# Performance work log

Measured on AMD Instinct MI355X. Metric: run time of the kernel, lower is better.

The kernel has to match this reference:

```python
import jax, jax.numpy as jnp
import numpy as np

ADAPT_RATE = 0.05


def setup_inputs() -> dict:
    key = jax.random.key(0)
    k1, k2, k3 = jax.random.split(key, 3)
    B, T, DIN, DOUT = 64, 256, 1024, 1024
    x = jax.random.normal(k1, (B, T, DIN), dtype=jnp.float32)
    W = jax.random.normal(k2, (DOUT, DIN), dtype=jnp.float32) / np.sqrt(DIN)
    b = jax.random.normal(k3, (DOUT,), dtype=jnp.float32) * 0.01
    threshold = jnp.ones((DOUT,), dtype=jnp.float32)
    return {"x": x, "W": W, "b": b, "threshold": threshold}


def reference(x, W, b, threshold):
    # Precompute the per-timestep linear once as a single big GEMM: [B,T,O]
    pre = jnp.einsum('bti,oi->bto', x, W) + b
    B, T, O = pre.shape

    def step(carry, pre_t):
        mem, thr = carry
        mem = mem + pre_t                       # membrane accumulate [B,O]
        s = (mem >= thr).astype(pre_t.dtype)    # hard threshold spike
        # adaptive threshold: in-place .data update in torch (no grad path)
        thr = thr + ADAPT_RATE * (s.mean(axis=0) - 0.5)
        mem = mem * (1.0 - s)                   # reset where spiked
        return (mem, thr), s

    mem0 = jnp.zeros((B, O), dtype=x.dtype)
    (_, _), spikes = jax.lax.scan(step, (mem0, threshold), jnp.swapaxes(pre, 0, 1))
    return jnp.swapaxes(spikes, 0, 1)  # [B,T,O]
```

## Files before the change

kernel.cpp:

```cpp
#include <hip/hip_runtime.h>

#define B_ 64
#define T_ 256
#define DIN_ 1024
#define DOUT_ 1024

typedef int v4i  __attribute__((ext_vector_type(4)));
typedef int v16i __attribute__((ext_vector_type(16)));

#define PRE_BYTES 134217728ULL
#define XS_BYTES  83886080ULL
#define WSL_BYTES 5242880ULL
#define SPM_BYTES 2097152ULL

__global__ __launch_bounds__(256) void snn_split_x(
    const float* __restrict__ x, char* __restrict__ xs)
{
    const int W    = blockIdx.x * 4 + (threadIdx.x >> 6);
    const int lane = threadIdx.x & 63;
    const int mt = W & 1, kt = (W >> 1) & 31, t0 = W >> 6;
    const int m = lane & 31, kh = lane >> 5;
    const int b = mt * 32 + m;

    const float* src = x + ((size_t)b * T_ + t0) * DIN_ + kt * 32 + kh * 16;
    float f[16];
    *(float4*)(f)      = *(const float4*)(src);
    *(float4*)(f + 4)  = *(const float4*)(src + 4);
    *(float4*)(f + 8)  = *(const float4*)(src + 8);
    *(float4*)(f + 12) = *(const float4*)(src + 12);

    unsigned pk[4][4];
#pragma unroll
    for (int s = 0; s < 4; ++s)
        pk[s][0] = pk[s][1] = pk[s][2] = pk[s][3] = 0u;
#pragma unroll
    for (int j = 0; j < 16; ++j) {
        float v = f[j] * 0.125f;
#pragma unroll
        for (int s = 0; s < 4; ++s) {
            const float ml = (s == 0) ? 64.f : 128.f;
            const float sv = __builtin_rintf(v * ml);
            v = v * ml - sv;
            const int iv = (int)sv;
            pk[s][j >> 2] |= ((unsigned)iv & 0xffu) << ((j & 3) * 8);
        }
    }
#pragma unroll
    for (int s = 0; s < 4; ++s) {
        char* dst = xs + (size_t)(((s * 256 + t0) * 32 + kt) * 2 + mt) * 1024
                       + lane * 16;
        *(uint4*)dst = make_uint4(pk[s][0], pk[s][1], pk[s][2], pk[s][3]);
    }
}

__global__ __launch_bounds__(256) void snn_split_w(
    const float* __restrict__ Wt, char* __restrict__ wsl)
{
    const int W    = blockIdx.x * 4 + (threadIdx.x >> 6);
    const int lane = threadIdx.x & 63;
    const int kt = W & 31, ot = W >> 5;
    const int n = lane & 31, kh = lane >> 5;
    const int o = ot * 32 + n;

    const float* src = Wt + (size_t)o * DIN_ + kt * 32 + kh * 16;
    float f[16];
    *(float4*)(f)      = *(const float4*)(src);
    *(float4*)(f + 4)  = *(const float4*)(src + 4);
    *(float4*)(f + 8)  = *(const float4*)(src + 8);
    *(float4*)(f + 12) = *(const float4*)(src + 12);

    unsigned pk[4][4];
#pragma unroll
    for (int s = 0; s < 4; ++s)
        pk[s][0] = pk[s][1] = pk[s][2] = pk[s][3] = 0u;
#pragma unroll
    for (int j = 0; j < 16; ++j) {
        float v = f[j] * 4.0f;
#pragma unroll
        for (int s = 0; s < 4; ++s) {
            const float ml = (s == 0) ? 64.f : 128.f;
            const float sv = __builtin_rintf(v * ml);
            v = v * ml - sv;
            const int iv = (int)sv;
            pk[s][j >> 2] |= ((unsigned)iv & 0xffu) << ((j & 3) * 8);
        }
    }
#pragma unroll
    for (int s = 0; s < 4; ++s) {
        char* dst = wsl + (size_t)((s * 32 + ot) * 32 + kt) * 1024 + lane * 16;
        *(uint4*)dst = make_uint4(pk[s][0], pk[s][1], pk[s][2], pk[s][3]);
    }
}

__global__ __launch_bounds__(256, 3) void snn_gemm_i8(
    const char* __restrict__ xs, const char* __restrict__ wsl,
    const float* __restrict__ bias, double* __restrict__ pre)
{
    const int t0 = blockIdx.x >> 4;
    const int oc = blockIdx.x & 15;
    const int tid = threadIdx.x;
    const int lane = tid & 63;
    const int ws = __builtin_amdgcn_readfirstlane(tid >> 6);
    const int wm = ws >> 1;
    const int wo = ws & 1;
    const int lo = lane * 16;

    v16i acc[4];
#pragma unroll
    for (int g = 0; g < 4; ++g)
#pragma unroll
        for (int r = 0; r < 16; ++r) acc[g][r] = 0;

    const char* ab = xs  + (size_t)(t0 * 64 + wm) * 1024 + lo;
    const char* bb = wsl + (size_t)((oc * 2 + wo) * 32) * 1024 + lo;

    v4i aP[4], bP[4], aQ[4], bQ[4];

#define LOAD_A(R, KT)                                                          \
    do { _Pragma("unroll")                                                     \
        for (int s = 0; s < 4; ++s)                                            \
            R[s] = *(const v4i*)(ab + (size_t)s * 16777216 +                   \
                                 (size_t)(KT) * 2048);                         \
    } while (0)
#define LOAD_B(R, KT)                                                          \
    do { _Pragma("unroll")                                                     \
        for (int s = 0; s < 4; ++s)                                            \
            R[s] = *(const v4i*)(bb + (size_t)s * 1048576 +                    \
                                 (size_t)(KT) * 1024);                         \
    } while (0)
#define MFMA10(A, B)                                                           \
    do {                                                                       \
        __builtin_amdgcn_s_setprio(1);                                         \
        acc[3] = __builtin_amdgcn_mfma_i32_32x32x32_i8(A[0], B[3], acc[3],0,0,0);\
        acc[2] = __builtin_amdgcn_mfma_i32_32x32x32_i8(A[0], B[2], acc[2],0,0,0);\
        acc[1] = __builtin_amdgcn_mfma_i32_32x32x32_i8(A[0], B[1], acc[1],0,0,0);\
        acc[3] = __builtin_amdgcn_mfma_i32_32x32x32_i8(A[1], B[2], acc[3],0,0,0);\
        acc[2] = __builtin_amdgcn_mfma_i32_32x32x32_i8(A[1], B[1], acc[2],0,0,0);\
        acc[1] = __builtin_amdgcn_mfma_i32_32x32x32_i8(A[1], B[0], acc[1],0,0,0);\
        acc[3] = __builtin_amdgcn_mfma_i32_32x32x32_i8(A[2], B[1], acc[3],0,0,0);\
        acc[2] = __builtin_amdgcn_mfma_i32_32x32x32_i8(A[2], B[0], acc[2],0,0,0);\
        acc[0] = __builtin_amdgcn_mfma_i32_32x32x32_i8(A[0], B[0], acc[0],0,0,0);\
        acc[3] = __builtin_amdgcn_mfma_i32_32x32x32_i8(A[3], B[0], acc[3],0,0,0);\
        __builtin_amdgcn_s_setprio(0);                                         \
    } while (0)

    LOAD_A(aP, 0); LOAD_B(bP, 0);
    for (int ks = 0; ks < 15; ++ks) {
        const int kt = 2 * ks;
        LOAD_A(aQ, kt + 1); LOAD_B(bQ, kt + 1);
        MFMA10(aP, bP);
        LOAD_A(aP, kt + 2); LOAD_B(bP, kt + 2);
        MFMA10(aQ, bQ);
    }
    LOAD_A(aQ, 31); LOAD_B(bQ, 31);
    MFMA10(aP, bP);
    MFMA10(aQ, bQ);

#undef LOAD_A
#undef LOAD_B
#undef MFMA10

    const int n = lane & 31, lh = lane >> 5;
    const int o = oc * 64 + wo * 32 + n;
    const double bv = (double)bias[o];
    double* dst = pre + ((size_t)t0 * DOUT_ + o) * 64 + wm * 32;
#pragma unroll
    for (int r = 0; r < 16; ++r) {
        const int row = (r & 3) + 8 * (r >> 2) + 4 * lh;
        double v = (double)acc[3][r];
        v = v * 0.0078125 + (double)acc[2][r];
        v = v * 0.0078125 + (double)acc[1][r];
        v = v * 0.0078125 + (double)acc[0][r];
        dst[row] = v * 0x1p-11 + bv;
    }
}

__global__ __launch_bounds__(256, 2) void snn_gemm_fb(
    const float* __restrict__ x, const float* __restrict__ W,
    const float* __restrict__ bias, double* __restrict__ pre)
{
    __shared__ float smem[2][8 * 72 + 8 * 256];
    const int t0 = blockIdx.x & 255;
    const int o0 = blockIdx.x >> 8;
    const int tid = threadIdx.x;
    const int to = tid & 31;
    const int tb = tid >> 5;

    double acc[8][8];
#pragma unroll
    for (int i = 0; i < 8; ++i)
#pragma unroll
        for (int j = 0; j < 8; ++j) acc[i][j] = 0.0;

    const int arow = tid >> 2;
    const int ak2  = (tid & 3) * 2;
    const float* xg = x + (size_t)(t0 + 256 * arow) * DIN_ + ak2;
    const float* wg = W + (size_t)(o0 * 256 + tid) * DIN_;

    float2 f2  = *(const float2*)(xg);
    float4 bq0 = *(const float4*)(wg);
    float4 bq1 = *(const float4*)(wg + 4);

    for (int kc = 0; kc < DIN_ / 8; ++kc) {
        float* base = smem[kc & 1];
        float (*AsF)[72]  = (float(*)[72])base;
        float (*BsF)[256] = (float(*)[256])(base + 8 * 72);
        AsF[ak2 + 0][arow] = f2.x;
        AsF[ak2 + 1][arow] = f2.y;
        BsF[0][tid] = bq0.x;  BsF[1][tid] = bq0.y;
        BsF[2][tid] = bq0.z;  BsF[3][tid] = bq0.w;
        BsF[4][tid] = bq1.x;  BsF[5][tid] = bq1.y;
        BsF[6][tid] = bq1.z;  BsF[7][tid] = bq1.w;
        __syncthreads();
        if (kc + 1 < DIN_ / 8) {
            f2  = *(const float2*)(xg + (kc + 1) * 8);
            bq0 = *(const float4*)(wg + (kc + 1) * 8);
            bq1 = *(const float4*)(wg + (kc + 1) * 8 + 4);
        }
#pragma unroll
        for (int k = 0; k < 8; ++k) {
            const float4 af0 = *(const float4*)&AsF[k][tb * 8];
            const float4 af1 = *(const float4*)&AsF[k][tb * 8 + 4];
            const float4 bf0 = *(const float4*)&BsF[k][to * 4];
            const float4 bf1 = *(const float4*)&BsF[k][128 + to * 4];
            double a[8], b[8];
            a[0] = (double)af0.x; a[1] = (double)af0.y;
            a[2] = (double)af0.z; a[3] = (double)af0.w;
            a[4] = (double)af1.x; a[5] = (double)af1.y;
            a[6] = (double)af1.z; a[7] = (double)af1.w;
            b[0] = (double)bf0.x; b[1] = (double)bf0.y;
            b[2] = (double)bf0.z; b[3] = (double)bf0.w;
            b[4] = (double)bf1.x; b[5] = (double)bf1.y;
            b[6] = (double)bf1.z; b[7] = (double)bf1.w;
#pragma unroll
            for (int i = 0; i < 8; ++i)
#pragma unroll
                for (int j = 0; j < 8; ++j)
                    acc[i][j] += a[i] * b[j];
        }
        __syncthreads();
    }

    double biasd[8];
#pragma unroll
    for (int j = 0; j < 8; ++j)
        biasd[j] = (double)bias[o0 * 256 + (j >> 2) * 128 + to * 4 + (j & 3)];
    double (*trans)[67] = (double(*)[67])smem[0];
    for (int c = 0; c < 16; ++c) {
        __syncthreads();
        const int j4  = c >> 3;
        const int tlo = (c & 7) * 4;
        if (to >= tlo && to < tlo + 4) {
#pragma unroll
            for (int p4 = 0; p4 < 4; ++p4) {
                const int r = (to - tlo) * 4 + p4;
                const int j = j4 * 4 + p4;
#pragma unroll
                for (int i = 0; i < 8; ++i)
                    trans[r][tb * 8 + i] = acc[i][j] + biasd[j];
            }
        }
        __syncthreads();
#pragma unroll
        for (int q = 0; q < 4; ++q) {
            const int idx = tid + 256 * q;
            const int b  = idx & 63;
            const int oc = idx >> 6;
            pre[(size_t)(t0 * DOUT_ + o0 * 256 + c * 16 + oc) * 64 + b] = trans[oc][b];
        }
    }
}

#define SCAN_LOAD(PV, TB)                                                      \
    do {                                                                       \
        _Pragma("unroll")                                                      \
        for (int j = 0; j < 16; ++j)                                           \
            PV[j] = p[(size_t)((TB) + j) * (DOUT_ * 64)];                      \
    } while (0)

#define SCAN_STEP(PV, TB)                                                      \
    do {                                                                       \
        _Pragma("unroll")                                                      \
        for (int j = 0; j < 16; ++j) {                                         \
            mem += PV[j];                                                      \
            const bool s = (mem >= thr);                                       \
            const unsigned long long msk = __ballot(s);                        \
            thr += 0.05 * ((double)__popcll(msk) * (1.0 / 64.0) - 0.5);        \
            if (spM) {                                                         \
                if (lane == 0) spM[(size_t)((TB) + j) * DOUT_ + o] = msk;      \
            } else {                                                           \
                outD[(size_t)lane * (T_ * DOUT_) +                             \
                     (size_t)((TB) + j) * DOUT_ + o] = s ? 1.0f : 0.0f;        \
            }                                                                  \
            mem = s ? 0.0 : mem;                                               \
        }                                                                      \
    } while (0)

__global__ __launch_bounds__(256) void snn_scan(
    const double* __restrict__ pre, const float* __restrict__ thr_in,
    unsigned long long* __restrict__ spM, float* __restrict__ outD)
{
    const int wid  = (blockIdx.x * blockDim.x + threadIdx.x) >> 6;
    const int lane = threadIdx.x & 63;
    if (wid >= DOUT_) return;
    const int o = wid;

    double mem = 0.0;
    double thr = (double)thr_in[o];
    const double* p = pre + (size_t)o * 64 + lane;

    double pvA[16], pvB[16];
    SCAN_LOAD(pvA, 0);
    for (int t = 0; t < T_; t += 32) {
        if (t + 16 < T_) SCAN_LOAD(pvB, t + 16);
        SCAN_STEP(pvA, t);
        if (t + 32 < T_) SCAN_LOAD(pvA, t + 32);
        SCAN_STEP(pvB, t + 16);
    }
}

__global__ __launch_bounds__(256) void snn_expand(
    const unsigned long long* __restrict__ spM, float* __restrict__ out)
{
    const int idx = blockIdx.x * 256 + threadIdx.x;
    const int og = idx & 255;
    const int t  = idx >> 8;
    const unsigned long long* mp = spM + (size_t)t * DOUT_ + og * 4;
    const unsigned long long m0 = mp[0], m1 = mp[1], m2 = mp[2], m3 = mp[3];
    float* op = out + (size_t)t * DOUT_ + og * 4;
#pragma unroll
    for (int b = 0; b < 64; ++b) {
        float4 v;
        v.x = (float)((m0 >> b) & 1ULL);
        v.y = (float)((m1 >> b) & 1ULL);
        v.z = (float)((m2 >> b) & 1ULL);
        v.w = (float)((m3 >> b) & 1ULL);
        *(float4*)(op + (size_t)b * (T_ * DOUT_)) = v;
    }
}

extern "C" void kernel_launch(void* const* d_in, const int* in_sizes, int n_in,
                              void* d_out, int out_size, void* d_ws, size_t ws_size,
                              hipStream_t stream) {
    const float* x    = (const float*)d_in[0];
    const float* W    = (const float*)d_in[1];
    const float* bias = (const float*)d_in[2];
    const float* thr  = (const float*)d_in[3];
    float* out = (float*)d_out;

    double* pre = (double*)d_ws;
    const size_t need = PRE_BYTES + XS_BYTES + WSL_BYTES + SPM_BYTES;

    if (ws_size >= need) {
        char* xs  = (char*)d_ws + PRE_BYTES;
        char* wsl = xs + XS_BYTES;
        unsigned long long* spM = (unsigned long long*)(wsl + WSL_BYTES);
        snn_split_x<<<4096, 256, 0, stream>>>(x, xs);
        snn_split_w<<<256, 256, 0, stream>>>(W, wsl);
        snn_gemm_i8<<<4096, 256, 0, stream>>>(xs, wsl, bias, pre);
        snn_scan<<<256, 256, 0, stream>>>(pre, thr, spM, nullptr);
        snn_expand<<<256, 256, 0, stream>>>(spM, out);
    } else {
        const bool two_stage = (ws_size >= PRE_BYTES + SPM_BYTES);
        unsigned long long* spM =
            two_stage ? (unsigned long long*)((char*)d_ws + PRE_BYTES) : nullptr;
        snn_gemm_fb<<<1024, 256, 0, stream>>>(x, W, bias, pre);
        snn_scan<<<256, 256, 0, stream>>>(pre, thr, spM, two_stage ? nullptr : out);
        if (two_stage)
            snn_expand<<<1024, 256, 0, stream>>>(spM, out);
    }
}
```

Measured before the change: 372.7 us.

## Stage W slices through LDS via async global_load_lds with triple buffering

The int8 GEMM now loads B (weight) tiles cooperatively into a three-stage LDS ring buffer using global_load_lds async copies, instead of each wave loading its own B fragments from global memory. Waves that share the same weight columns now read them from LDS, which cuts redundant global and L2 traffic. In exchange it adds a workgroup barrier and manual vmcnt waits every k-step. It also uses 24KB of LDS per block, which may limit occupancy.

```diff
diff --git a/kernel.cpp b/kernel.cpp
--- a/kernel.cpp
+++ b/kernel.cpp
@@ -12,6 +12,12 @@
 #define XS_BYTES  83886080ULL
 #define WSL_BYTES 5242880ULL
 #define SPM_BYTES 2097152ULL
+
+__device__ __forceinline__ void async_copy16(const void* g, void* l) {
+    __builtin_amdgcn_global_load_lds(
+        (const __attribute__((address_space(1))) void*)g,
+        (__attribute__((address_space(3))) void*)l, 16, 0, 0);
+}
 
 __global__ __launch_bounds__(256) void snn_split_x(
     const float* __restrict__ x, char* __restrict__ xs)
@@ -96,6 +102,7 @@
     const char* __restrict__ xs, const char* __restrict__ wsl,
     const float* __restrict__ bias, double* __restrict__ pre)
 {
+    __shared__ __align__(16) char ldsB[3][8 * 1024];
     const int t0 = blockIdx.x >> 4;
     const int oc = blockIdx.x & 15;
     const int tid = threadIdx.x;
@@ -111,10 +118,15 @@
 #pragma unroll
         for (int r = 0; r < 16; ++r) acc[g][r] = 0;
 
-    const char* ab = xs  + (size_t)(t0 * 64 + wm) * 1024 + lo;
-    const char* bb = wsl + (size_t)((oc * 2 + wo) * 32) * 1024 + lo;
-
-    v4i aP[4], bP[4], aQ[4], bQ[4];
+    const char* ab = xs + (size_t)(t0 * 64 + wm) * 1024 + lo;
+
+    const int c0 = ws * 2, c1 = ws * 2 + 1;
+    const char* sgB0 = wsl + (size_t)(c0 & 3) * 1048576
+                           + (size_t)(oc * 2 + (c0 >> 2)) * 32768 + lo;
+    const char* sgB1 = wsl + (size_t)(c1 & 3) * 1048576
+                           + (size_t)(oc * 2 + (c1 >> 2)) * 32768 + lo;
+
+    v4i aP[4], aQ[4];
 
 #define LOAD_A(R, KT)                                                          \
     do { _Pragma("unroll")                                                     \
@@ -122,11 +134,10 @@
             R[s] = *(const v4i*)(ab + (size_t)s * 16777216 +                   \
                                  (size_t)(KT) * 2048);                         \
     } while (0)
-#define LOAD_B(R, KT)                                                          \
-    do { _Pragma("unroll")                                                     \
-        for (int s = 0; s < 4; ++s)                                            \
-            R[s] = *(const v4i*)(bb + (size_t)s * 1048576 +                    \
-                                 (size_t)(KT) * 1024);                         \
+#define STAGE(JB, BUF)                                                         \
+    do {                                                                       \
+        async_copy16(sgB0 + (size_t)(JB) * 1024, &ldsB[BUF][c0 * 1024]);       \
+        async_copy16(sgB1 + (size_t)(JB) * 1024, &ldsB[BUF][c1 * 1024]);       \
     } while (0)
 #define MFMA10(A, B)                                                           \
     do {                                                                       \
@@ -143,22 +154,37 @@
         acc[3] = __builtin_amdgcn_mfma_i32_32x32x32_i8(A[3], B[0], acc[3],0,0,0);\
         __builtin_amdgcn_s_setprio(0);                                         \
     } while (0)
-
-    LOAD_A(aP, 0); LOAD_B(bP, 0);
-    for (int ks = 0; ks < 15; ++ks) {
-        const int kt = 2 * ks;
-        LOAD_A(aQ, kt + 1); LOAD_B(bQ, kt + 1);
-        MFMA10(aP, bP);
-        LOAD_A(aP, kt + 2); LOAD_B(bP, kt + 2);
-        MFMA10(aQ, bQ);
-    }
-    LOAD_A(aQ, 31); LOAD_B(bQ, 31);
-    MFMA10(aP, bP);
-    MFMA10(aQ, bQ);
-
+#define INTERVAL(KT, ACUR, ANXT)                                               \
+    do {                                                                       \
+        if ((KT) < 31) asm volatile("s_waitcnt vmcnt(2)" ::: "memory");        \
+        else           asm volatile("s_waitcnt vmcnt(0)" ::: "memory");        \
+        __builtin_amdgcn_s_barrier();                                          \
+        asm volatile("" ::: "memory");                                         \
+        if ((KT) + 1 < 32) LOAD_A(ANXT, (KT) + 1);                             \
+        if ((KT) + 2 < 32) STAGE((KT) + 2, st);                                \
+        const char* bufB = ldsB[rd];                                           \
+        v4i b[4];                                                              \
+        _Pragma("unroll")                                                      \
+        for (int s = 0; s < 4; ++s)                                            \
+            b[s] = *(const v4i*)(bufB + (wo * 4 + s) * 1024 + lo);             \
+        MFMA10(ACUR, b);                                                       \
+        rd = (rd == 2) ? 0 : rd + 1;                                           \
+        st = (st == 2) ? 0 : st + 1;                                           \
+    } while (0)
+
+    LOAD_A(aP, 0);
+    STAGE(0, 0);
+    STAGE(1, 1);
+
+    int rd = 0, st = 2;
+    for (int ks = 0; ks < 16; ++ks) {
+        INTERVAL(2 * ks,     aP, aQ);
+        INTERVAL(2 * ks + 1, aQ, aP);
+    }
+#undef INTERVAL
+#undef MFMA10
+#undef STAGE
 #undef LOAD_A
-#undef LOAD_B
-#undef MFMA10
 
     const int n = lane & 31, lh = lane >> 5;
     const int o = oc * 64 + wo * 32 + n;
```

Measured after the change: 347.6 us. 6.7% less time.
